# Kernel tuning notes

Hardware: AMD Instinct MI355X
Metric: run time of the kernel (lower is better)

Reference implementation:

```python
import jax, jax.numpy as jnp
import numpy as np

B, S, D, H = 2, 2048, 768, 12
DH = D // H


def setup_inputs() -> dict:
    key = jax.random.key(0)
    ks = jax.random.split(key, 12)
    f32 = jnp.float32
    sd = 1.0 / np.sqrt(D)
    return {
        "q": jax.random.normal(ks[0], (B, S, D), f32),
        "k": jax.random.normal(ks[1], (B, S, D), f32),
        "v": jax.random.normal(ks[2], (B, S, D), f32),
        "mask": jax.random.normal(ks[3], (S, S), f32),
        "Wq": jax.random.normal(ks[4], (D, D), f32) * sd,
        "bq": jnp.zeros((D,), f32),
        "Wk": jax.random.normal(ks[5], (D, D), f32) * sd,
        "bk": jnp.zeros((D,), f32),
        "Wv": jax.random.normal(ks[6], (D, D), f32) * sd,
        "bv": jnp.zeros((D,), f32),
        "Wo": jax.random.normal(ks[7], (D, D), f32) * sd,
        "bo": jnp.zeros((D,), f32),
    }


def reference(q, k, v, mask, Wq, bq, Wk, bk, Wv, bv, Wo, bo):
    # torch nn.Linear: y = x @ W.T + b
    qh = (q @ Wq.T + bq).reshape(B, S, H, DH).transpose(0, 2, 1, 3)  # [B,H,S,DH]
    kh = (k @ Wk.T + bk).reshape(B, S, H, DH).transpose(0, 2, 1, 3)
    vh = (v @ Wv.T + bv).reshape(B, S, H, DH).transpose(0, 2, 1, 3)
    scores = jnp.einsum("bhsd,bhtd->bhst", qh, kh)  # [B,H,S,S]
    # original adds mask after permute to [H,B,S,S]; with an [S,S] mask the
    # broadcast add is identical either way
    scores = scores + mask
    attn = jax.nn.softmax(scores.astype(jnp.float32) / np.sqrt(DH), axis=-1)
    out = jnp.einsum("bhst,bhtd->bhsd", attn, vh)  # [B,H,S,DH]
    out = out.transpose(0, 2, 1, 3).reshape(B, S, D)
    return out @ Wo.T + bo
```

## Files before the change

kernel.cpp:

```cpp
#include <hip/hip_runtime.h>
#include <hip/hip_bf16.h>

#define B_ 2
#define S_ 2048
#define D_ 768
#define H_ 12
#define DH_ 64
#define M_ (B_*S_)
#define BH_ (B_*H_)

typedef __bf16 v8bf __attribute__((ext_vector_type(8)));
typedef __bf16 v4bf __attribute__((ext_vector_type(4)));
typedef float  v4f  __attribute__((ext_vector_type(4)));

static __device__ __forceinline__ v4f mfma16(v8bf a, v8bf b, v4f c) {
  return __builtin_amdgcn_mfma_f32_16x16x32_bf16(a, b, c, 0, 0, 0);
}

static __device__ __forceinline__ void gload_lds16(const __bf16* g, __bf16* l) {
  __builtin_amdgcn_global_load_lds(
      (const __attribute__((address_space(1))) unsigned int*)g,
      (__attribute__((address_space(3))) unsigned int*)l,
      16, 0, 0);
}

#define C1_ 0.18033688011112042f

__global__ __launch_bounds__(256) void convert_kernel(
    const float* __restrict__ q, const float* __restrict__ k, const float* __restrict__ v,
    const float* __restrict__ Wq, const float* __restrict__ Wk,
    const float* __restrict__ Wv, const float* __restrict__ Wo,
    __bf16* __restrict__ Xq, __bf16* __restrict__ Xk, __bf16* __restrict__ Xv,
    __bf16* __restrict__ Wqb, __bf16* __restrict__ Wkb,
    __bf16* __restrict__ Wvb, __bf16* __restrict__ Wob)
{
  const float* src; __bf16* dst; int n;
  switch (blockIdx.y) {
    case 0: src = q;  dst = Xq;  n = M_*D_; break;
    case 1: src = k;  dst = Xk;  n = M_*D_; break;
    case 2: src = v;  dst = Xv;  n = M_*D_; break;
    case 3: src = Wq; dst = Wqb; n = D_*D_; break;
    case 4: src = Wk; dst = Wkb; n = D_*D_; break;
    case 5: src = Wv; dst = Wvb; n = D_*D_; break;
    default: src = Wo; dst = Wob; n = D_*D_; break;
  }
  int n4 = n >> 2;
  for (int i = blockIdx.x*blockDim.x + threadIdx.x; i < n4; i += gridDim.x*blockDim.x) {
    float4 x = ((const float4*)src)[i];
    v4bf y;
    y[0] = (__bf16)x.x; y[1] = (__bf16)x.y; y[2] = (__bf16)x.z; y[3] = (__bf16)x.w;
    ((v4bf*)dst)[i] = y;
  }
}

__global__ __launch_bounds__(256) void em_kernel(
    const float* __restrict__ mask, __bf16* __restrict__ em)
{
  int t = blockIdx.x*256 + threadIdx.x;
  int L = t & 63; int rest = t >> 6;
  int w = rest & 7; rest >>= 3;
  int kt = rest & 63; rest >>= 6;
  int qt = rest;
  int row = qt*128 + w*16 + (L & 15);
  int key0 = kt*32 + ((L >> 4) << 2);
  const float* mp = mask + (size_t)row*S_ + key0;
  float4 m0 = *(const float4*)mp;
  float4 m1 = *(const float4*)(mp + 16);
  v8bf e;
  e[0] = (__bf16)exp2f(C1_*m0.x); e[1] = (__bf16)exp2f(C1_*m0.y);
  e[2] = (__bf16)exp2f(C1_*m0.z); e[3] = (__bf16)exp2f(C1_*m0.w);
  e[4] = (__bf16)exp2f(C1_*m1.x); e[5] = (__bf16)exp2f(C1_*m1.y);
  e[6] = (__bf16)exp2f(C1_*m1.z); e[7] = (__bf16)exp2f(C1_*m1.w);
  *(v8bf*)(em + (size_t)t*8) = e;
}

template<int BM, int BN>
static __device__ __forceinline__ void gemm_core_lds(
    const __bf16* __restrict__ A, const __bf16* __restrict__ W,
    int m0, int n0, __bf16* lds, v4f acc[BM/32][BN/32])
{
  constexpr int NFA = BM/16, NFB = BN/16;
  constexpr int PW  = (NFA + NFB) / 4;
  constexpr int MI  = BM/32, NJ = BN/32;
  const int lane = threadIdx.x & 63;
  const int wave = threadIdx.x >> 6;
  const int r16 = lane & 15;
  const int kc8 = (lane >> 4) << 3;
  const int ia = (wave >> 1) * MI;
  const int ib = (wave & 1) * NJ;

  const __bf16* gsrc[PW]; __bf16* ldst[PW];
  #pragma unroll
  for (int t = 0; t < PW; t++) {
    int fb = wave*PW + t;
    gsrc[t] = (fb < NFA)
        ? A + (size_t)(m0 + fb*16 + r16)*D_ + kc8
        : W + (size_t)(n0 + (fb - NFA)*16 + r16)*D_ + kc8;
    ldst[t] = lds + fb*512;
  }

  for (int k0 = 0; k0 < D_; k0 += 32) {
    #pragma unroll
    for (int t = 0; t < PW; t++) gload_lds16(gsrc[t] + k0, ldst[t]);
    __syncthreads();
    v8bf a[MI], b[NJ];
    #pragma unroll
    for (int i = 0; i < MI; i++) a[i] = *(const v8bf*)(lds + (ia+i)*512 + lane*8);
    #pragma unroll
    for (int j = 0; j < NJ; j++) b[j] = *(const v8bf*)(lds + (NFA+ib+j)*512 + lane*8);
    #pragma unroll
    for (int i = 0; i < MI; i++)
      #pragma unroll
      for (int j = 0; j < NJ; j++)
        acc[i][j] = mfma16(a[i], b[j], acc[i][j]);
    __syncthreads();
  }
}

__global__ __launch_bounds__(256) void qkv_gemm(
    const __bf16* __restrict__ Xq, const __bf16* __restrict__ Xk, const __bf16* __restrict__ Xv,
    const __bf16* __restrict__ Wqb, const __bf16* __restrict__ Wkb, const __bf16* __restrict__ Wvb,
    const float* __restrict__ bq, const float* __restrict__ bk, const float* __restrict__ bv,
    __bf16* __restrict__ qf, __bf16* __restrict__ kf, __bf16* __restrict__ vf)
{
  __shared__ __bf16 lds[(128+64)*32];
  const int mode = blockIdx.z;
  const __bf16* A = (mode == 0) ? Xq : (mode == 1) ? Xk : Xv;
  const __bf16* W = (mode == 0) ? Wqb : (mode == 1) ? Wkb : Wvb;
  const float* bias = (mode == 0) ? bq : (mode == 1) ? bk : bv;
  const int m0 = blockIdx.y << 7, n0 = blockIdx.x << 6;
  v4f acc[4][2];
  #pragma unroll
  for (int i = 0; i < 4; i++)
    #pragma unroll
    for (int j = 0; j < 2; j++) { v4f z = {0.f,0.f,0.f,0.f}; acc[i][j] = z; }
  gemm_core_lds<128,64>(A, W, m0, n0, lds, acc);

  const int lane = threadIdx.x & 63;
  const int wave = threadIdx.x >> 6;
  const int wm = (wave >> 1) << 6, wn = (wave & 1) << 5;
  const int col = lane & 15, quad = lane >> 4;
  float bb[2]; int nn[2];
  #pragma unroll
  for (int j = 0; j < 2; j++) { nn[j] = n0 + wn + 16*j + col; bb[j] = bias[nn[j]]; }

  if (mode < 2) {
    __bf16* dst = (mode == 0) ? qf : kf;
    const float sc = (mode == 0) ? C1_ : 1.0f;
    #pragma unroll
    for (int i = 0; i < 4; i++)
      #pragma unroll
      for (int r = 0; r < 4; r++) {
        int m = m0 + wm + 16*i + quad*4 + r;
        int batch = m >> 11, s = m & (S_-1);
        #pragma unroll
        for (int j = 0; j < 2; j++) {
          int n = nn[j];
          int h = n >> 6, dd = n & 63;
          size_t flat = (((size_t)(batch*H_ + h)*128 + (s >> 4))*2 + (dd >> 5))*512
                      + ((((dd >> 3) & 3)*16 + (s & 15)) << 3) + (dd & 7);
          dst[flat] = (__bf16)((acc[i][j][r] + bb[j]) * sc);
        }
      }
  } else {
    #pragma unroll
    for (int i = 0; i < 4; i++) {
      int mbase = m0 + wm + 16*i + quad*4;
      int batch = mbase >> 11, s0 = mbase & (S_-1);
      #pragma unroll
      for (int j = 0; j < 2; j++) {
        int n = nn[j];
        int h = n >> 6, dd = n & 63;
        v4bf pk;
        #pragma unroll
        for (int r = 0; r < 4; r++) pk[r] = (__bf16)(acc[i][j][r] + bb[j]);
        size_t flat = (((size_t)(batch*H_ + h)*64 + (s0 >> 5))*4 + (dd >> 4))*512
                    + ((((s0 >> 3) & 3)*16 + (dd & 15)) << 3) + (s0 & 7);
        *(v4bf*)(vf + flat) = pk;
      }
    }
  }
}

__global__ __launch_bounds__(512, 2) void attn_kernel(
    const __bf16* __restrict__ qf, const __bf16* __restrict__ kf, const __bf16* __restrict__ vf,
    const __bf16* __restrict__ em, __bf16* __restrict__ ao)
{
  __shared__ __bf16 kv[4][2][2048];
  __shared__ __bf16 plds[8][16][40];

  const int bh = blockIdx.y;
  const int qt = blockIdx.x;
  const int wave = threadIdx.x >> 6, lane = threadIdx.x & 63;
  const int col = lane & 15, quad = lane >> 4, koff = quad << 3;
  const int batch = bh / H_, h = bh % H_;
  const __bf16* qfb = qf + (size_t)bh * (S_*DH_);
  const __bf16* kfb = kf + (size_t)bh * (S_*DH_);
  const __bf16* vfb = vf + (size_t)bh * (S_*DH_);
  const __bf16* emw = em + (size_t)qt * 262144 + wave*512 + lane*8;
  __bf16 (*pt)[40] = plds[wave];

  const __bf16* gsrc = ((wave < 4) ? kfb : vfb) + ((wave & 3) << 9) + lane*8;
  __bf16* kvd[4];
  #pragma unroll
  for (int b = 0; b < 4; b++) kvd[b] = &kv[b][wave >> 2][(wave & 3) << 9];

  const __bf16* qblk = qfb + (size_t)(qt*8 + wave)*1024;
  v8bf Qf0 = *(const v8bf*)(qblk + lane*8);
  v8bf Qf1 = *(const v8bf*)(qblk + 512 + lane*8);

  v4f O[4];
  #pragma unroll
  for (int f = 0; f < 4; f++) { v4f z = {0.f,0.f,0.f,0.f}; O[f] = z; }
  float li = 0.f;

  asm volatile("" ::: "memory");
  gload_lds16(gsrc, kvd[0]);
  v8bf ef0 = *(const v8bf*)(emw);
  asm volatile("" ::: "memory");
  gload_lds16(gsrc + 2048, kvd[1]);
  v8bf ef1 = *(const v8bf*)(emw + 4096);
  v8bf ef2, ef3;

#define ATT_STEP(P, EFC, EFN, ISSUE, WSTR) \
  { \
    asm volatile("s_waitcnt vmcnt(" WSTR ")" ::: "memory"); \
    __builtin_amdgcn_s_barrier(); \
    asm volatile("" ::: "memory"); \
    if (ISSUE) { \
      const int nkt = kt0 + (P) + 2; \
      gload_lds16(gsrc + (size_t)nkt*2048, kvd[((P)+2)&3]); \
      EFN = *(const v8bf*)(emw + (size_t)nkt*4096); \
    } \
    const __bf16* Kb = kv[(P)&3][0]; \
    const __bf16* Vb = kv[(P)&3][1]; \
    v8bf Ka0 = *(const v8bf*)(Kb + lane*8); \
    v8bf Ka1 = *(const v8bf*)(Kb + 512 + lane*8); \
    v8bf Ka2 = *(const v8bf*)(Kb + 1024 + lane*8); \
    v8bf Ka3 = *(const v8bf*)(Kb + 1536 + lane*8); \
    v4f s0 = {0.f,0.f,0.f,0.f}, s1 = {0.f,0.f,0.f,0.f}; \
    s0 = mfma16(Ka0, Qf0, s0); s0 = mfma16(Ka1, Qf1, s0); \
    s1 = mfma16(Ka2, Qf0, s1); s1 = mfma16(Ka3, Qf1, s1); \
    float p[8], rs = 0.f; \
    _Pragma("unroll") \
    for (int j = 0; j < 4; j++) { \
      p[j]   = exp2f(s0[j]) * (float)EFC[j]; \
      p[4+j] = exp2f(s1[j]) * (float)EFC[4+j]; \
    } \
    _Pragma("unroll") \
    for (int j = 0; j < 8; j++) rs += p[j]; \
    li += rs; \
    v4bf pk0, pk1; \
    _Pragma("unroll") \
    for (int r = 0; r < 4; r++) { pk0[r] = (__bf16)p[r]; pk1[r] = (__bf16)p[4+r]; } \
    *(v4bf*)(&pt[col][quad*4])      = pk0; \
    *(v4bf*)(&pt[col][16 + quad*4]) = pk1; \
    v8bf Pf = *(const v8bf*)(&pt[col][koff]); \
    v8bf Vf0 = *(const v8bf*)(Vb + lane*8); \
    v8bf Vf1 = *(const v8bf*)(Vb + 512 + lane*8); \
    v8bf Vf2 = *(const v8bf*)(Vb + 1024 + lane*8); \
    v8bf Vf3 = *(const v8bf*)(Vb + 1536 + lane*8); \
    O[0] = mfma16(Vf0, Pf, O[0]); \
    O[1] = mfma16(Vf1, Pf, O[1]); \
    O[2] = mfma16(Vf2, Pf, O[2]); \
    O[3] = mfma16(Vf3, Pf, O[3]); \
  }

  #pragma unroll 1
  for (int kt0 = 0; kt0 < 60; kt0 += 4) {
    ATT_STEP(0, ef0, ef2, true, "2");
    ATT_STEP(1, ef1, ef3, true, "2");
    ATT_STEP(2, ef2, ef0, true, "2");
    ATT_STEP(3, ef3, ef1, true, "2");
  }
  {
    const int kt0 = 60;
    ATT_STEP(0, ef0, ef2, true,  "2");
    ATT_STEP(1, ef1, ef3, true,  "2");
    ATT_STEP(2, ef2, ef0, false, "2");
    ATT_STEP(3, ef3, ef1, false, "0");
  }
#undef ATT_STEP

  float rs = li;
  rs += __shfl_xor(rs, 16);
  rs += __shfl_xor(rs, 32);
  float invl = 1.f / rs;
  const int qg = (qt << 7) + (wave << 4) + col;
  __bf16* orow = ao + ((size_t)batch*S_ + qg)*D_ + h*DH_ + quad*4;
  #pragma unroll
  for (int f = 0; f < 4; f++) {
    v4bf o;
    #pragma unroll
    for (int r = 0; r < 4; r++) o[r] = (__bf16)(O[f][r] * invl);
    *(v4bf*)(orow + f*16) = o;
  }
}

__global__ __launch_bounds__(256) void out_gemm(
    const __bf16* __restrict__ Ao, const __bf16* __restrict__ Wob,
    const float* __restrict__ bo, float* __restrict__ out)
{
  __shared__ __bf16 lds[(64+64)*32];
  const int m0 = blockIdx.y << 6, n0 = blockIdx.x << 6;
  v4f acc[2][2];
  #pragma unroll
  for (int i = 0; i < 2; i++)
    #pragma unroll
    for (int j = 0; j < 2; j++) { v4f z = {0.f,0.f,0.f,0.f}; acc[i][j] = z; }
  gemm_core_lds<64,64>(Ao, Wob, m0, n0, lds, acc);

  const int lane = threadIdx.x & 63;
  const int wave = threadIdx.x >> 6;
  const int wm = (wave >> 1) << 5, wn = (wave & 1) << 5;
  const int col = lane & 15, quad = lane >> 4;
  float bb[2]; int nn[2];
  #pragma unroll
  for (int j = 0; j < 2; j++) { nn[j] = n0 + wn + 16*j + col; bb[j] = bo[nn[j]]; }
  #pragma unroll
  for (int i = 0; i < 2; i++)
    #pragma unroll
    for (int r = 0; r < 4; r++) {
      int m = m0 + wm + 16*i + quad*4 + r;
      #pragma unroll
      for (int j = 0; j < 2; j++)
        out[(size_t)m*D_ + nn[j]] = acc[i][j][r] + bb[j];
    }
}

extern "C" void kernel_launch(void* const* d_in, const int* in_sizes, int n_in,
                              void* d_out, int out_size, void* d_ws, size_t ws_size,
                              hipStream_t stream)
{
  const float* q    = (const float*)d_in[0];
  const float* k    = (const float*)d_in[1];
  const float* v    = (const float*)d_in[2];
  const float* mask = (const float*)d_in[3];
  const float* Wq   = (const float*)d_in[4];
  const float* bq   = (const float*)d_in[5];
  const float* Wk   = (const float*)d_in[6];
  const float* bk   = (const float*)d_in[7];
  const float* Wv   = (const float*)d_in[8];
  const float* bv   = (const float*)d_in[9];
  const float* Wo   = (const float*)d_in[10];
  const float* bo   = (const float*)d_in[11];

  const size_t XN = (size_t)M_ * D_;
  const size_t WN = (size_t)D_ * D_;
  const size_t HN = (size_t)BH_ * S_ * DH_;

  char* ws = (char*)d_ws;
  __bf16* Xq  = (__bf16*)ws;                 ws += XN * 2;
  __bf16* Xk  = (__bf16*)ws;                 ws += XN * 2;
  __bf16* Xv  = (__bf16*)ws;                 ws += XN * 2;
  __bf16* Wqb = (__bf16*)ws;                 ws += WN * 2;
  __bf16* Wkb = (__bf16*)ws;                 ws += WN * 2;
  __bf16* Wvb = (__bf16*)ws;                 ws += WN * 2;
  __bf16* Wob = (__bf16*)ws;                 ws += WN * 2;
  __bf16* qfb = (__bf16*)ws;                 ws += HN * 2;
  __bf16* kfb = (__bf16*)ws;                 ws += HN * 2;
  __bf16* vfb = (__bf16*)ws;                 ws += HN * 2;
  __bf16* aob = (__bf16*)ws;                 ws += XN * 2;
  __bf16* emb = Xq;

  convert_kernel<<<dim3(3072, 7), 256, 0, stream>>>(
      q, k, v, Wq, Wk, Wv, Wo, Xq, Xk, Xv, Wqb, Wkb, Wvb, Wob);
  qkv_gemm<<<dim3(12, 32, 3), 256, 0, stream>>>(
      Xq, Xk, Xv, Wqb, Wkb, Wvb, bq, bk, bv, qfb, kfb, vfb);
  em_kernel<<<dim3(2048), 256, 0, stream>>>(mask, emb);
  attn_kernel<<<dim3(16, 24), 512, 0, stream>>>(qfb, kfb, vfb, emb, aob);
  out_gemm<<<dim3(12, 64), 256, 0, stream>>>(aob, Wob, bo, (float*)d_out);
}
```

Measured before the change: 253.1 us.

## Use 128x128 tiles with triple-buffered async LDS pipeline in both GEMMs

Replaces the generic single-buffered GEMM core with a 128x128-tile routine that keeps three LDS buffers in flight. It issues global-to-LDS loads two k-steps ahead and waits with explicit vmcnt counters plus one barrier per step, so load latency overlaps with MFMA work. The QKV and output GEMM grids shrink to match the larger tiles, and the convert kernel grid is reduced. The risks are fewer blocks for the small output GEMM, which may leave compute units idle, and higher register and LDS use per block.

Measured after the change: 239.5 us. 5.4% less time.

```diff
diff --git a/kernel.cpp b/kernel.cpp
--- a/kernel.cpp
+++ b/kernel.cpp
@@ -74,75 +74,98 @@
   *(v8bf*)(em + (size_t)t*8) = e;
 }
 
-template<int BM, int BN>
-static __device__ __forceinline__ void gemm_core_lds(
+static __device__ __forceinline__ void gemm128_pipe(
     const __bf16* __restrict__ A, const __bf16* __restrict__ W,
-    int m0, int n0, __bf16* lds, v4f acc[BM/32][BN/32])
-{
-  constexpr int NFA = BM/16, NFB = BN/16;
-  constexpr int PW  = (NFA + NFB) / 4;
-  constexpr int MI  = BM/32, NJ = BN/32;
+    int m0, int n0, __bf16* lds, v4f acc[4][4])
+{
   const int lane = threadIdx.x & 63;
   const int wave = threadIdx.x >> 6;
   const int r16 = lane & 15;
   const int kc8 = (lane >> 4) << 3;
-  const int ia = (wave >> 1) * MI;
-  const int ib = (wave & 1) * NJ;
-
-  const __bf16* gsrc[PW]; __bf16* ldst[PW];
-  #pragma unroll
-  for (int t = 0; t < PW; t++) {
-    int fb = wave*PW + t;
-    gsrc[t] = (fb < NFA)
+  const int ia = (wave >> 1) << 2;
+  const int ib = (wave & 1) << 2;
+
+  const __bf16* gsrc[4]; int ldo[4];
+  #pragma unroll
+  for (int t = 0; t < 4; t++) {
+    int fb = wave*4 + t;
+    gsrc[t] = (fb < 8)
         ? A + (size_t)(m0 + fb*16 + r16)*D_ + kc8
-        : W + (size_t)(n0 + (fb - NFA)*16 + r16)*D_ + kc8;
-    ldst[t] = lds + fb*512;
-  }
-
-  for (int k0 = 0; k0 < D_; k0 += 32) {
-    #pragma unroll
-    for (int t = 0; t < PW; t++) gload_lds16(gsrc[t] + k0, ldst[t]);
-    __syncthreads();
-    v8bf a[MI], b[NJ];
-    #pragma unroll
-    for (int i = 0; i < MI; i++) a[i] = *(const v8bf*)(lds + (ia+i)*512 + lane*8);
-    #pragma unroll
-    for (int j = 0; j < NJ; j++) b[j] = *(const v8bf*)(lds + (NFA+ib+j)*512 + lane*8);
-    #pragma unroll
-    for (int i = 0; i < MI; i++)
-      #pragma unroll
-      for (int j = 0; j < NJ; j++)
-        acc[i][j] = mfma16(a[i], b[j], acc[i][j]);
-    __syncthreads();
-  }
-}
-
-__global__ __launch_bounds__(256) void qkv_gemm(
+        : W + (size_t)(n0 + (fb - 8)*16 + r16)*D_ + kc8;
+    ldo[t] = fb << 9;
+  }
+
+  asm volatile("" ::: "memory");
+  #pragma unroll
+  for (int t = 0; t < 4; t++) gload_lds16(gsrc[t], lds + ldo[t]);
+  asm volatile("" ::: "memory");
+  #pragma unroll
+  for (int t = 0; t < 4; t++) gload_lds16(gsrc[t] + 32, lds + 8192 + ldo[t]);
+  asm volatile("" ::: "memory");
+
+#define G_STEP(CUR, NXTB, KC, ISSUE, WSTR) { \
+    asm volatile("s_waitcnt vmcnt(" WSTR ")" ::: "memory"); \
+    __builtin_amdgcn_s_barrier(); \
+    asm volatile("" ::: "memory"); \
+    if (ISSUE) { \
+      _Pragma("unroll") \
+      for (int t = 0; t < 4; t++) \
+        gload_lds16(gsrc[t] + (KC), lds + (NXTB)*8192 + ldo[t]); \
+    } \
+    const __bf16* buf = lds + (CUR)*8192; \
+    v8bf a[4], b[4]; \
+    _Pragma("unroll") \
+    for (int i = 0; i < 4; i++) a[i] = *(const v8bf*)(buf + ((ia+i) << 9) + lane*8); \
+    _Pragma("unroll") \
+    for (int j = 0; j < 4; j++) b[j] = *(const v8bf*)(buf + ((8+ib+j) << 9) + lane*8); \
+    _Pragma("unroll") \
+    for (int i = 0; i < 4; i++) \
+      _Pragma("unroll") \
+      for (int j = 0; j < 4; j++) \
+        acc[i][j] = mfma16(a[i], b[j], acc[i][j]); \
+  }
+
+  #pragma unroll 1
+  for (int ks0 = 0; ks0 < 18; ks0 += 3) {
+    G_STEP(0, 2, (ks0+2)*32, true, "4");
+    G_STEP(1, 0, (ks0+3)*32, true, "4");
+    G_STEP(2, 1, (ks0+4)*32, true, "4");
+  }
+  G_STEP(0, 2, 20*32, true,  "4");
+  G_STEP(1, 0, 21*32, true,  "4");
+  G_STEP(2, 1, 22*32, true,  "4");
+  G_STEP(0, 2, 23*32, true,  "4");
+  G_STEP(1, 0, 0,     false, "4");
+  G_STEP(2, 0, 0,     false, "0");
+#undef G_STEP
+}
+
+__global__ __launch_bounds__(256, 3) void qkv_gemm(
     const __bf16* __restrict__ Xq, const __bf16* __restrict__ Xk, const __bf16* __restrict__ Xv,
     const __bf16* __restrict__ Wqb, const __bf16* __restrict__ Wkb, const __bf16* __restrict__ Wvb,
     const float* __restrict__ bq, const float* __restrict__ bk, const float* __restrict__ bv,
     __bf16* __restrict__ qf, __bf16* __restrict__ kf, __bf16* __restrict__ vf)
 {
-  __shared__ __bf16 lds[(128+64)*32];
+  __shared__ __bf16 lds[3*8192];
   const int mode = blockIdx.z;
   const __bf16* A = (mode == 0) ? Xq : (mode == 1) ? Xk : Xv;
   const __bf16* W = (mode == 0) ? Wqb : (mode == 1) ? Wkb : Wvb;
   const float* bias = (mode == 0) ? bq : (mode == 1) ? bk : bv;
-  const int m0 = blockIdx.y << 7, n0 = blockIdx.x << 6;
-  v4f acc[4][2];
+  const int m0 = blockIdx.y << 7, n0 = blockIdx.x << 7;
+  v4f acc[4][4];
   #pragma unroll
   for (int i = 0; i < 4; i++)
     #pragma unroll
-    for (int j = 0; j < 2; j++) { v4f z = {0.f,0.f,0.f,0.f}; acc[i][j] = z; }
-  gemm_core_lds<128,64>(A, W, m0, n0, lds, acc);
+    for (int j = 0; j < 4; j++) { v4f z = {0.f,0.f,0.f,0.f}; acc[i][j] = z; }
+  gemm128_pipe(A, W, m0, n0, lds, acc);
 
   const int lane = threadIdx.x & 63;
   const int wave = threadIdx.x >> 6;
-  const int wm = (wave >> 1) << 6, wn = (wave & 1) << 5;
+  const int wm = (wave >> 1) << 6, wn = (wave & 1) << 6;
   const int col = lane & 15, quad = lane >> 4;
-  float bb[2]; int nn[2];
-  #pragma unroll
-  for (int j = 0; j < 2; j++) { nn[j] = n0 + wn + 16*j + col; bb[j] = bias[nn[j]]; }
+  float bb[4]; int nn[4];
+  #pragma unroll
+  for (int j = 0; j < 4; j++) { nn[j] = n0 + wn + 16*j + col; bb[j] = bias[nn[j]]; }
 
   if (mode < 2) {
     __bf16* dst = (mode == 0) ? qf : kf;
@@ -154,7 +177,7 @@
         int m = m0 + wm + 16*i + quad*4 + r;
         int batch = m >> 11, s = m & (S_-1);
         #pragma unroll
-        for (int j = 0; j < 2; j++) {
+        for (int j = 0; j < 4; j++) {
           int n = nn[j];
           int h = n >> 6, dd = n & 63;
           size_t flat = (((size_t)(batch*H_ + h)*128 + (s >> 4))*2 + (dd >> 5))*512
@@ -168,7 +191,7 @@
       int mbase = m0 + wm + 16*i + quad*4;
       int batch = mbase >> 11, s0 = mbase & (S_-1);
       #pragma unroll
-      for (int j = 0; j < 2; j++) {
+      for (int j = 0; j < 4; j++) {
         int n = nn[j];
         int h = n >> 6, dd = n & 63;
         v4bf pk;
@@ -297,33 +320,33 @@
   }
 }
 
-__global__ __launch_bounds__(256) void out_gemm(
+__global__ __launch_bounds__(256, 3) void out_gemm(
     const __bf16* __restrict__ Ao, const __bf16* __restrict__ Wob,
     const float* __restrict__ bo, float* __restrict__ out)
 {
-  __shared__ __bf16 lds[(64+64)*32];
-  const int m0 = blockIdx.y << 6, n0 = blockIdx.x << 6;
-  v4f acc[2][2];
-  #pragma unroll
-  for (int i = 0; i < 2; i++)
-    #pragma unroll
-    for (int j = 0; j < 2; j++) { v4f z = {0.f,0.f,0.f,0.f}; acc[i][j] = z; }
-  gemm_core_lds<64,64>(Ao, Wob, m0, n0, lds, acc);
+  __shared__ __bf16 lds[3*8192];
+  const int m0 = blockIdx.y << 7, n0 = blockIdx.x << 7;
+  v4f acc[4][4];
+  #pragma unroll
+  for (int i = 0; i < 4; i++)
+    #pragma unroll
+    for (int j = 0; j < 4; j++) { v4f z = {0.f,0.f,0.f,0.f}; acc[i][j] = z; }
+  gemm128_pipe(Ao, Wob, m0, n0, lds, acc);
 
   const int lane = threadIdx.x & 63;
   const int wave = threadIdx.x >> 6;
-  const int wm = (wave >> 1) << 5, wn = (wave & 1) << 5;
+  const int wm = (wave >> 1) << 6, wn = (wave & 1) << 6;
   const int col = lane & 15, quad = lane >> 4;
-  float bb[2]; int nn[2];
-  #pragma unroll
-  for (int j = 0; j < 2; j++) { nn[j] = n0 + wn + 16*j + col; bb[j] = bo[nn[j]]; }
-  #pragma unroll
-  for (int i = 0; i < 2; i++)
+  float bb[4]; int nn[4];
+  #pragma unroll
+  for (int j = 0; j < 4; j++) { nn[j] = n0 + wn + 16*j + col; bb[j] = bo[nn[j]]; }
+  #pragma unroll
+  for (int i = 0; i < 4; i++)
     #pragma unroll
     for (int r = 0; r < 4; r++) {
       int m = m0 + wm + 16*i + quad*4 + r;
       #pragma unroll
-      for (int j = 0; j < 2; j++)
+      for (int j = 0; j < 4; j++)
         out[(size_t)m*D_ + nn[j]] = acc[i][j][r] + bb[j];
     }
 }
@@ -363,11 +386,11 @@
   __bf16* aob = (__bf16*)ws;                 ws += XN * 2;
   __bf16* emb = Xq;
 
-  convert_kernel<<<dim3(3072, 7), 256, 0, stream>>>(
+  convert_kernel<<<dim3(768, 7), 256, 0, stream>>>(
       q, k, v, Wq, Wk, Wv, Wo, Xq, Xk, Xv, Wqb, Wkb, Wvb, Wob);
-  qkv_gemm<<<dim3(12, 32, 3), 256, 0, stream>>>(
+  qkv_gemm<<<dim3(6, 32, 3), 256, 0, stream>>>(
       Xq, Xk, Xv, Wqb, Wkb, Wvb, bq, bk, bv, qfb, kfb, vfb);
   em_kernel<<<dim3(2048), 256, 0, stream>>>(mask, emb);
   attn_kernel<<<dim3(16, 24), 512, 0, stream>>>(qfb, kfb, vfb, emb, aob);
-  out_gemm<<<dim3(12, 64), 256, 0, stream>>>(aob, Wob, bo, (float*)d_out);
-}
+  out_gemm<<<dim3(6, 32), 256, 0, stream>>>(aob, Wob, bo, (float*)d_out);
+}
```
